# Kernel optimization log

Hardware: AMD Instinct MI355X
Metric: run time of the kernel (lower is better)

## Reference

```python
import jax, jax.numpy as jnp
import numpy as np

B, C, D, T = 8, 512, 256, 2048
EPS = 1e-5


def setup_inputs() -> dict:
    key = jax.random.key(0)
    ks = jax.random.split(key, 9)
    s_c = 1.0 / np.sqrt(C)
    s_d = 1.0 / np.sqrt(D)
    return {
        "inpt": jax.random.normal(ks[0], (B, C, T), dtype=jnp.float32),
        "theta_w": jax.random.uniform(ks[1], (D, C), jnp.float32, -s_c, s_c),
        "theta_b": jax.random.uniform(ks[2], (D,), jnp.float32, -s_c, s_c),
        "phi_w": jax.random.uniform(ks[3], (D, C), jnp.float32, -s_c, s_c),
        "phi_b": jax.random.uniform(ks[4], (D,), jnp.float32, -s_c, s_c),
        "g_w": jax.random.uniform(ks[5], (D, C), jnp.float32, -s_c, s_c),
        "g_b": jax.random.uniform(ks[6], (D,), jnp.float32, -s_c, s_c),
        "ht_w": jax.random.uniform(ks[7], (C, D), jnp.float32, -s_d, s_d),
        "ht_b": jax.random.uniform(ks[8], (C,), jnp.float32, -s_d, s_d),
        "bn_gamma": jnp.ones((C,), dtype=jnp.float32),
        "bn_beta": jnp.zeros((C,), dtype=jnp.float32),
    }


def reference(inpt, theta_w, theta_b, phi_w, phi_b, g_w, g_b, ht_w, ht_b, bn_gamma, bn_beta):
    # 1x1 convs are just channel-mixing matmuls: (B,C,T) -> (B,D,T)
    theta = jnp.einsum('dc,bct->bdt', theta_w, inpt) + theta_b[None, :, None]
    phi = jnp.einsum('dc,bct->bdt', phi_w, inpt) + phi_b[None, :, None]
    g = jnp.einsum('dc,bct->bdt', g_w, inpt) + g_b[None, :, None]
    # w[b,t,s] = sum_d theta[b,d,t] * phi[b,d,s]; softmax over s (phi time)
    w = jnp.einsum('bdt,bds->bts', theta, phi)
    w = jax.nn.softmax(w, axis=-1)
    # torch.matmul(g, w): out[b,d,s] = sum_t g[b,d,t] * w[b,t,s]
    attn = jnp.einsum('bdt,bts->bds', g, w)
    # ht 1x1 conv back to C channels
    h = jnp.einsum('cd,bdt->bct', ht_w, attn) + ht_b[None, :, None]
    # BatchNorm1d in training mode: batch stats over (B, T) per channel
    mean = jnp.mean(h, axis=(0, 2), keepdims=True)
    var = jnp.var(h, axis=(0, 2), keepdims=True)  # biased variance
    h_norm = (h - mean) * jax.lax.rsqrt(var + EPS)
    bn = bn_gamma[None, :, None] * h_norm + bn_beta[None, :, None]
    return inpt + bn
```

## Files before the change

### kernel.cpp

```cpp
#include <hip/hip_runtime.h>
#include <hip/hip_bf16.h>
#include <math.h>

#define Bx 8
#define Cx 512
#define Dx 256
#define Tx 2048
#define EPSx 1e-5f

typedef _Float16 h16;
typedef __attribute__((ext_vector_type(8))) _Float16 h16x8;
typedef __attribute__((ext_vector_type(8))) short s16x8;
typedef __attribute__((ext_vector_type(4))) float f32x4;

typedef __attribute__((address_space(3))) unsigned int lds_u32;
typedef __attribute__((address_space(1))) const unsigned int glb_u32;

__device__ __forceinline__ void cp16(void* ldsp, const void* g) {
    __builtin_amdgcn_global_load_lds((glb_u32*)g, (lds_u32*)ldsp, 16, 0, 0);
}

template<int MODE, bool BF, int TN>
__global__ __launch_bounds__(256, 4)
void gemm_mf(const h16* __restrict__ A, long aBatch, int lda,
             const h16* __restrict__ B, long bBatch, int ldb,
             void* __restrict__ C, long cBatch, int ldc,
             float* __restrict__ Cp, float* __restrict__ Z,
             int M, int N, int K, int mBlk,
             const float* __restrict__ biasM, const float* __restrict__ biasN) {
    constexpr int NJ = TN / 32;
    __shared__ h16 As[128 * 64];
    __shared__ h16 Bs[TN * 64];
    const int tid  = threadIdx.x;
    const int lane = tid & 63, wid = tid >> 6;
    const int wm = (wid & 1) * 64, wn = (wid >> 1) * (TN / 2);
    const int lm = lane & 15, quad = lane >> 4;
    const unsigned id = blockIdx.x;
    const int b = id & 7;
    const unsigned rr = id >> 3;
    const int m0 = (rr % (unsigned)mBlk) * 128;
    const int n0 = (rr / (unsigned)mBlk) * TN;
    const h16* Ab = A + (size_t)b * aBatch + (size_t)m0 * lda;
    const h16* Bb = B + (size_t)b * bBatch + (size_t)n0 * ldb;

    const int srow  = tid >> 3;
    const int sclog = (tid & 7) ^ (srow & 7);
    char* ldsA = (char*)As + (tid & ~63) * 16;
    char* ldsB = (char*)Bs + (tid & ~63) * 16;

    f32x4 acc[4][NJ] = {};

    for (int k0 = 0; k0 < K; k0 += 64) {
        __syncthreads();
#pragma unroll
        for (int i = 0; i < 4; i++) {
            int r = srow + 32 * i;
            cp16(ldsA + i * 4096, Ab + (size_t)r * lda + k0 + sclog * 8);
        }
#pragma unroll
        for (int i = 0; i < TN / 32; i++) {
            int r = srow + 32 * i;
            cp16(ldsB + i * 4096, Bb + (size_t)r * ldb + k0 + sclog * 8);
        }
        __syncthreads();
#pragma unroll
        for (int ks = 0; ks < 2; ks++) {
            s16x8 af[4], bf4[NJ];
#pragma unroll
            for (int i = 0; i < 4; i++) {
                int row = wm + 16 * i + lm;
                int st = (ks * 4 + quad) ^ (lm & 7);
                af[i] = *(const s16x8*)(As + row * 64 + st * 8);
            }
#pragma unroll
            for (int j = 0; j < NJ; j++) {
                int row = wn + 16 * j + lm;
                int st = (ks * 4 + quad) ^ (lm & 7);
                bf4[j] = *(const s16x8*)(Bs + row * 64 + st * 8);
            }
#pragma unroll
            for (int i = 0; i < 4; i++)
#pragma unroll
                for (int j = 0; j < NJ; j++) {
                    if constexpr (BF)
                        acc[i][j] = __builtin_amdgcn_mfma_f32_16x16x32_bf16(
                            af[i], bf4[j], acc[i][j], 0, 0, 0);
                    else
                        acc[i][j] = __builtin_amdgcn_mfma_f32_16x16x32_f16(
                            __builtin_bit_cast(h16x8, af[i]),
                            __builtin_bit_cast(h16x8, bf4[j]), acc[i][j], 0, 0, 0);
                }
        }
    }

    if constexpr (MODE == 0) {
        h16* Cb = (h16*)C + (size_t)b * cBatch;
#pragma unroll
        for (int i = 0; i < 4; i++)
#pragma unroll
            for (int j = 0; j < NJ; j++) {
                int row = m0 + wm + 16 * i + quad * 4;
                int col = n0 + wn + 16 * j + lm;
                float bN = biasN ? biasN[col] : 0.0f;
#pragma unroll
                for (int r = 0; r < 4; r++) {
                    float v = acc[i][j][r] + bN;
                    if (biasM) v += biasM[row + r];
                    Cb[(size_t)(row + r) * ldc + col] = (h16)v;
                }
            }
    } else if constexpr (MODE == 1) {
        __hip_bfloat16* Cb = (__hip_bfloat16*)C + (size_t)b * cBatch;
#pragma unroll
        for (int j = 0; j < NJ; j++) {
            int col = n0 + wn + 16 * j + lm;
            float iz = 1.0f / Z[(size_t)b * N + col];
#pragma unroll
            for (int i = 0; i < 4; i++) {
                int row = m0 + wm + 16 * i + quad * 4;
#pragma unroll
                for (int r = 0; r < 4; r++)
                    Cb[(size_t)(row + r) * ldc + col] =
                        __float2bfloat16(acc[i][j][r] * iz);
            }
        }
    } else if constexpr (MODE == 2) {
        __syncthreads();
        float* Zl = (float*)As;
        if (tid < TN) Zl[tid] = 0.0f;
        __syncthreads();
        __hip_bfloat16* Cb = (__hip_bfloat16*)C + (size_t)b * cBatch;
#pragma unroll
        for (int j = 0; j < NJ; j++) {
            int cl = wn + 16 * j + lm;
            int col = n0 + cl;
            float zp = 0.0f;
#pragma unroll
            for (int i = 0; i < 4; i++) {
                int row = m0 + wm + 16 * i + quad * 4;
#pragma unroll
                for (int r = 0; r < 4; r++) {
                    float e = __expf(acc[i][j][r]);
                    zp += e;
                    Cb[(size_t)(row + r) * ldc + col] = __float2bfloat16(e);
                }
            }
            atomicAdd(&Zl[cl], zp);
        }
        __syncthreads();
        if (tid < TN) atomicAdd(&Z[(size_t)b * N + n0 + tid], Zl[tid]);
    } else {
        __syncthreads();
        float* Sl = (float*)As;
        float* Sq = Sl + TN;
        if (tid < 2 * TN) Sl[tid] = 0.0f;
        __syncthreads();
        h16* Cb = (h16*)C + (size_t)b * cBatch;
#pragma unroll
        for (int j = 0; j < NJ; j++) {
            int cl = wn + 16 * j + lm;
            int col = n0 + cl;
            float bN = biasN[col];
            float s = 0.0f, q = 0.0f;
#pragma unroll
            for (int i = 0; i < 4; i++) {
                int row = m0 + wm + 16 * i + quad * 4;
#pragma unroll
                for (int r = 0; r < 4; r++) {
                    float v = acc[i][j][r] + bN;
                    s += v;
                    q = fmaf(v, v, q);
                    Cb[(size_t)(row + r) * ldc + col] = (h16)v;
                }
            }
            atomicAdd(&Sl[cl], s);
            atomicAdd(&Sq[cl], q);
        }
        __syncthreads();
        if (tid < TN) {
            atomicAdd(&Cp[n0 + tid], Sl[tid]);
            atomicAdd(&Z[n0 + tid], Sq[tid]);
        }
    }
}

__global__ __launch_bounds__(256)
void conv_prep(const float* __restrict__ inpt, h16* __restrict__ xT,
               const float* __restrict__ w0, const float* __restrict__ w1,
               const float* __restrict__ w2, const float* __restrict__ w3,
               const float* __restrict__ tb, const float* __restrict__ pb,
               const float* __restrict__ gb,
               h16* __restrict__ dst, float* __restrict__ bias3,
               float* __restrict__ Z, float* __restrict__ psum,
               float* __restrict__ pssq) {
    const int tid = threadIdx.x;
    if (blockIdx.z == 8) {
        int bx = blockIdx.y * 32 + blockIdx.x;
#pragma unroll
        for (int rep = 0; rep < 2; rep++) {
            int idx4 = bx * 512 + rep * 256 + tid;
            int arr = idx4 >> 15, local4 = idx4 & 32767;
            const float* srcs[4] = {w0, w1, w2, w3};
            float4 v = ((const float4*)srcs[arr])[local4];
            h16 o[4] = {(h16)v.x, (h16)v.y, (h16)v.z, (h16)v.w};
            *(uint2*)(dst + (size_t)arr * 131072 + (size_t)local4 * 4) = *(uint2*)o;
        }
        if (bx < 64) Z[bx * 256 + tid] = 0.0f;
        if (bx == 64) bias3[tid] = tb[tid];
        if (bx == 65) bias3[256 + tid] = pb[tid];
        if (bx == 66) bias3[512 + tid] = gb[tid];
        if (bx == 67) {
            psum[tid] = 0.0f; psum[tid + 256] = 0.0f;
            pssq[tid] = 0.0f; pssq[tid + 256] = 0.0f;
        }
        return;
    }
    __shared__ float lds[64][68];
    const int b = blockIdx.z;
    const int t0 = blockIdx.x * 64, c0 = blockIdx.y * 64;
    const int q = tid >> 4, k = tid & 15;
    const float* ib = inpt + (size_t)b * Cx * Tx;
#pragma unroll
    for (int i = 0; i < 4; i++) {
        int c = q + 16 * i;
        float4 v = *(const float4*)(ib + (size_t)(c0 + c) * Tx + t0 + 4 * k);
        *(float4*)&lds[c][4 * k] = v;
    }
    __syncthreads();
    h16* xb = xT + (size_t)b * Tx * Cx;
#pragma unroll
    for (int i = 0; i < 4; i++) {
        int t = q + 16 * i;
        h16 o[4];
#pragma unroll
        for (int j = 0; j < 4; j++) o[j] = (h16)lds[4 * k + j][t];
        *(uint2*)(xb + (size_t)(t0 + t) * Cx + c0 + 4 * k) = *(uint2*)o;
    }
}

__global__ __launch_bounds__(256)
void bn_apply_T(const float* __restrict__ inpt, const h16* __restrict__ hT,
                const float* __restrict__ psum, const float* __restrict__ pssq,
                const float* __restrict__ gamma, const float* __restrict__ beta,
                float* __restrict__ out) {
    __shared__ float lds[64][68];
    const int b = blockIdx.z, t0 = blockIdx.x * 64, c0 = blockIdx.y * 64;
    const int tid = threadIdx.x, q = tid >> 4, k = tid & 15;
    const h16* hb = hT + (size_t)b * Tx * Cx;
#pragma unroll
    for (int i = 0; i < 4; i++) {
        int t = q + 16 * i;
        uint2 raw = *(const uint2*)(hb + (size_t)(t0 + t) * Cx + c0 + 4 * k);
        const h16* hp = (const h16*)&raw;
        float4 v = make_float4((float)hp[0], (float)hp[1], (float)hp[2], (float)hp[3]);
        *(float4*)&lds[t][4 * k] = v;
    }
    __syncthreads();
    const float* ib = inpt + (size_t)b * Cx * Tx;
    float* ob = out + (size_t)b * Cx * Tx;
    const float invN = 1.0f / (float)(Bx * Tx);
#pragma unroll
    for (int i = 0; i < 4; i++) {
        int c = q + 16 * i;
        int cg = c0 + c;
        float mu = psum[cg] * invN;
        float var = pssq[cg] * invN - mu * mu;
        float rv = rsqrtf(var + EPSx);
        float ga = gamma[cg], be = beta[cg];
        float4 x = *(const float4*)(ib + (size_t)cg * Tx + t0 + 4 * k);
        float4 o;
        o.x = x.x + ga * (lds[4 * k + 0][c] - mu) * rv + be;
        o.y = x.y + ga * (lds[4 * k + 1][c] - mu) * rv + be;
        o.z = x.z + ga * (lds[4 * k + 2][c] - mu) * rv + be;
        o.w = x.w + ga * (lds[4 * k + 3][c] - mu) * rv + be;
        *(float4*)(ob + (size_t)cg * Tx + t0 + 4 * k) = o;
    }
}

extern "C" void kernel_launch(void* const* d_in, const int* in_sizes, int n_in,
                              void* d_out, int out_size, void* d_ws, size_t ws_size,
                              hipStream_t stream) {
    const float* inpt    = (const float*)d_in[0];
    const float* theta_w = (const float*)d_in[1];
    const float* theta_b = (const float*)d_in[2];
    const float* phi_w   = (const float*)d_in[3];
    const float* phi_b   = (const float*)d_in[4];
    const float* g_w     = (const float*)d_in[5];
    const float* g_b     = (const float*)d_in[6];
    const float* ht_w    = (const float*)d_in[7];
    const float* ht_b    = (const float*)d_in[8];
    const float* gamma   = (const float*)d_in[9];
    const float* beta    = (const float*)d_in[10];

    char* ws = (char*)d_ws;
    h16*   xT    = (h16*)(ws + 0);
    h16*   w4    = (h16*)(ws + 16777216);
    h16*   wHt   = w4 + 393216;
    float* bias3 = (float*)(ws + 17825792);
    float* Z     = (float*)(ws + 17828864);
    float* psum  = (float*)(ws + 17894400);
    float* pssq  = (float*)(ws + 17896448);
    h16*   thpg  = (h16*)(ws + 17902592);
    h16*   gh    = (h16*)(ws + 43068416);
    h16*   LT    = (h16*)(ws + 59845632);
    h16*   hT    = xT;

    const long sX  = (long)Tx * Cx;
    const long sTP = (long)Tx * 768;
    const long sGH = (long)Cx * Tx;
    const long sW  = (long)Tx * Tx;

    dim3 blk(256);
    conv_prep<<<dim3(Tx / 64, Cx / 64, Bx + 1), blk, 0, stream>>>(
        inpt, xT, theta_w, phi_w, g_w, ht_w, theta_b, phi_b, g_b,
        w4, bias3, Z, psum, pssq);
    gemm_mf<0, false, 128><<<dim3(768), blk, 0, stream>>>(
        xT, sX, Cx, w4, 0, Cx, thpg, sTP, 768, nullptr, nullptr,
        Tx, 768, Cx, 16, nullptr, bias3);
    gemm_mf<2, false, 128><<<dim3(2048), blk, 0, stream>>>(
        thpg + 256, sTP, 768, thpg, sTP, 768, LT, sW, Tx, nullptr, Z,
        Tx, Tx, Dx, 16, nullptr, nullptr);
    gemm_mf<1, false, 128><<<dim3(512), blk, 0, stream>>>(
        wHt, 0, Dx, thpg + 512, sTP, 768, gh, sGH, Tx, nullptr, Z,
        Cx, Tx, Dx, 4, nullptr, nullptr);
    gemm_mf<3, true, 64><<<dim3(1024), blk, 0, stream>>>(
        LT, sW, Tx, gh, sGH, Tx, hT, sX, Cx, psum, pssq,
        Tx, Cx, Tx, 16, nullptr, ht_b);
    bn_apply_T<<<dim3(Tx / 64, Cx / 64, Bx), blk, 0, stream>>>(
        inpt, hT, psum, pssq, gamma, beta, (float*)d_out);
}
```

Measured before the change: 223.0 us.

## Reassociate attention output: apply ht projection after attention, not before

Previously the ht 1x1 conv was folded into g first, giving a C-channel (512) operand, so the dominant T×T attention GEMM produced 512 output columns. Now g is computed separately at D=256 channels, with bias and the softmax 1/Z scaling folded into its epilogue. The T×T GEMM then produces only 256 columns, and the small ht projection runs afterwards with K=256. This roughly halves the FLOPs of the largest GEMM, at the cost of one more kernel launch and an extra intermediate buffer round-trip.

```diff
diff --git a/kernel.cpp b/kernel.cpp
--- a/kernel.cpp
+++ b/kernel.cpp
@@ -119,9 +119,11 @@
             for (int i = 0; i < 4; i++) {
                 int row = m0 + wm + 16 * i + quad * 4;
 #pragma unroll
-                for (int r = 0; r < 4; r++)
-                    Cb[(size_t)(row + r) * ldc + col] =
-                        __float2bfloat16(acc[i][j][r] * iz);
+                for (int r = 0; r < 4; r++) {
+                    float v = acc[i][j][r];
+                    if (biasM) v += biasM[row + r];
+                    Cb[(size_t)(row + r) * ldc + col] = __float2bfloat16(v * iz);
+                }
             }
         }
     } else if constexpr (MODE == 2) {
@@ -300,32 +302,37 @@
     float* Z     = (float*)(ws + 17828864);
     float* psum  = (float*)(ws + 17894400);
     float* pssq  = (float*)(ws + 17896448);
-    h16*   thpg  = (h16*)(ws + 17902592);
-    h16*   gh    = (h16*)(ws + 43068416);
-    h16*   LT    = (h16*)(ws + 59845632);
+    h16*   thph  = (h16*)(ws + 17902592);
+    h16*   gT    = (h16*)(ws + 34679808);
+    h16*   attn  = (h16*)(ws + 43068416);
+    h16*   LT    = (h16*)(ws + 51457024);
     h16*   hT    = xT;
 
     const long sX  = (long)Tx * Cx;
-    const long sTP = (long)Tx * 768;
-    const long sGH = (long)Cx * Tx;
+    const long sTP = (long)Tx * 512;
+    const long sGT = (long)Dx * Tx;
+    const long sAT = (long)Tx * Dx;
     const long sW  = (long)Tx * Tx;
 
     dim3 blk(256);
     conv_prep<<<dim3(Tx / 64, Cx / 64, Bx + 1), blk, 0, stream>>>(
         inpt, xT, theta_w, phi_w, g_w, ht_w, theta_b, phi_b, g_b,
         w4, bias3, Z, psum, pssq);
-    gemm_mf<0, false, 128><<<dim3(768), blk, 0, stream>>>(
-        xT, sX, Cx, w4, 0, Cx, thpg, sTP, 768, nullptr, nullptr,
-        Tx, 768, Cx, 16, nullptr, bias3);
+    gemm_mf<0, false, 128><<<dim3(512), blk, 0, stream>>>(
+        xT, sX, Cx, w4, 0, Cx, thph, sTP, 512, nullptr, nullptr,
+        Tx, 512, Cx, 16, nullptr, bias3);
     gemm_mf<2, false, 128><<<dim3(2048), blk, 0, stream>>>(
-        thpg + 256, sTP, 768, thpg, sTP, 768, LT, sW, Tx, nullptr, Z,
+        thph + 256, sTP, 512, thph, sTP, 512, LT, sW, Tx, nullptr, Z,
         Tx, Tx, Dx, 16, nullptr, nullptr);
-    gemm_mf<1, false, 128><<<dim3(512), blk, 0, stream>>>(
-        wHt, 0, Dx, thpg + 512, sTP, 768, gh, sGH, Tx, nullptr, Z,
-        Cx, Tx, Dx, 4, nullptr, nullptr);
-    gemm_mf<3, true, 64><<<dim3(1024), blk, 0, stream>>>(
-        LT, sW, Tx, gh, sGH, Tx, hT, sX, Cx, psum, pssq,
-        Tx, Cx, Tx, 16, nullptr, ht_b);
+    gemm_mf<1, false, 64><<<dim3(512), blk, 0, stream>>>(
+        w4 + 512 * 512, 0, Cx, xT, sX, Cx, gT, sGT, Tx, nullptr, Z,
+        Dx, Tx, Cx, 2, bias3 + 512, nullptr);
+    gemm_mf<0, true, 64><<<dim3(512), blk, 0, stream>>>(
+        LT, sW, Tx, gT, sGT, Tx, attn, sAT, Dx, nullptr, nullptr,
+        Tx, Dx, Tx, 16, nullptr, nullptr);
+    gemm_mf<3, false, 64><<<dim3(1024), blk, 0, stream>>>(
+        attn, sAT, Dx, wHt, 0, Dx, hT, sX, Cx, psum, pssq,
+        Tx, Cx, Dx, 16, nullptr, ht_b);
     bn_apply_T<<<dim3(Tx / 64, Cx / 64, Bx), blk, 0, stream>>>(
         inpt, hT, psum, pssq, gamma, beta, (float*)d_out);
 }
```

Result: faster. 216.8 us (-2.8%).
